# Optimization experiments

Measured on AMD Instinct MI355X. Metric: run time of the kernel, lower is better.

Reference implementation:

```python
import jax, jax.numpy as jnp
import numpy as np

B, N, H_DIM = 64, 128, 128
NODE_S, NODE_V = 64, 32            # irreps_node = 64x0e + 32x1o -> dim 160
OUT_S, OUT_V = 32, 16              # out irreps  = 32x0e + 16x1o -> dim 80
RBF, ZEMB, HID, LAT, EDIM, NE = 16, 32, 128, 256, 16, 512
EATT = 4096
CUTOFF = 5.0
MAXZ = 100
NODE_DIM = NODE_S + 3 * NODE_V
OUT_DIM = OUT_S + 3 * OUT_V
WN = NODE_S*OUT_S + NODE_V*OUT_S + NODE_S*OUT_V + NODE_V*OUT_V  # 4608 TP weights per edge
GATE_IN = H_DIM + H_DIM + RBF + 1

def _lin(k, fi, fo):
    return jax.random.normal(k, (fi, fo), jnp.float32) / np.sqrt(fi)

def setup_inputs() -> dict:
    ks = jax.random.split(jax.random.key(0), 24)
    flat = B * N
    att_dist = jax.random.uniform(ks[0], (EATT,), jnp.float32, 0.05, CUTOFF)
    dirs = jax.random.normal(ks[1], (EATT, 3), jnp.float32)
    dirs = dirs / jnp.linalg.norm(dirs, axis=-1, keepdims=True)
    return dict(
        h=jax.random.normal(ks[2], (B, N, H_DIM), jnp.float32),
        h_full=jax.random.normal(ks[3], (B, N, NODE_DIM), jnp.float32),
        z=jax.random.randint(ks[4], (B, N), 1, MAXZ + 1),
        mask=jnp.ones((B, N), bool),
        e_feat=jax.random.normal(ks[5], (NE, EDIM), jnp.float32),
        absorber_index=jax.random.randint(ks[6], (B,), 0, N),
        att_dst=jax.random.randint(ks[7], (EATT,), 0, flat),
        att_dist=att_dist,
        att_vec=dirs * att_dist[:, None],
        w_zemb=jax.random.normal(ks[8], (MAXZ + 1, ZEMB), jnp.float32),
        w1_rad=_lin(ks[9], ZEMB + 1 + RBF, HID), b1_rad=jnp.zeros(HID, jnp.float32),
        w2_rad=_lin(ks[10], HID, WN), b2_rad=jnp.zeros(WN, jnp.float32),
        wg1=_lin(ks[11], GATE_IN, HID), bg1=jnp.zeros(HID, jnp.float32),
        wg2=_lin(ks[12], HID, 1), bg2=jnp.zeros(1, jnp.float32),
        we1=_lin(ks[13], EDIM, HID), be1=jnp.zeros(HID, jnp.float32),
        we2=_lin(ks[14], HID, OUT_S + OUT_V), be2=jnp.ones(OUT_S + OUT_V, jnp.float32),
        wo1=_lin(ks[15], OUT_S + OUT_V, HID), bo1=jnp.zeros(HID, jnp.float32),
        wo2=_lin(ks[16], HID, HID), bo2=jnp.zeros(HID, jnp.float32),
        wo3=_lin(ks[17], HID, LAT), bo3=jnp.zeros(LAT, jnp.float32),
    )

def _core(h, h_full, z, e_feat, absorber_index, att_dst, att_dist, att_vec,
          w_zemb, w1_rad, b1_rad, w2_rad, b2_rad, wg1, bg1, wg2, bg2,
          we1, be1, we2, be2, wo1, bo1, wo2, bo2, wo3, bo3):
    B_, N_, H_ = h.shape
    flat = B_ * N_
    dt = h.dtype
    # scatter edge data into flat (B*N) buffers
    amask = jnp.zeros((flat,), bool).at[att_dst].set(True)
    dflat = jnp.zeros((flat,), dt).at[att_dst].set(att_dist.astype(dt))
    vflat = jnp.zeros((flat, 3), dt).at[att_dst].set(att_vec.astype(dt))
    eps = jnp.maximum(dflat, 1e-8)
    u = vflat / eps[:, None]
    # component-normalized real spherical harmonics, lmax=1: Y0 = 1, Y1 = sqrt(3)*u
    ys = jnp.ones((flat, 1), dt)
    yv = jnp.sqrt(jnp.asarray(3.0, dt)) * u
    # Gaussian RBF on distance
    centers = jnp.linspace(0.0, CUTOFF, RBF).astype(dt)
    width = CUTOFF / (RBF - 1)
    rbf = jnp.exp(-0.5 * ((dflat[:, None] - centers) / width) ** 2)
    zr = w_zemb[z].reshape(flat, ZEMB)
    is_abs = jax.nn.one_hot(absorber_index, N_, dtype=dt)  # (B,N)
    win = jnp.concatenate([zr, is_abs.reshape(flat, 1), rbf], -1)
    tpw = jax.nn.silu(win @ w1_rad + b1_rad) @ w2_rad + b2_rad  # (flat, WN)
    o = 0
    wA = tpw[:, o:o + NODE_S*OUT_S].reshape(flat, NODE_S, OUT_S); o += NODE_S*OUT_S
    wB = tpw[:, o:o + NODE_V*OUT_S].reshape(flat, NODE_V, OUT_S); o += NODE_V*OUT_S
    wC = tpw[:, o:o + NODE_S*OUT_V].reshape(flat, NODE_S, OUT_V); o += NODE_S*OUT_V
    wD = tpw[:, o:o + NODE_V*OUT_V].reshape(flat, NODE_V, OUT_V)
    hf = h_full.reshape(flat, NODE_DIM)
    s1 = hf[:, :NODE_S]
    v1 = hf[:, NODE_S:].reshape(flat, NODE_V, 3)
    norm = 1.0 / np.sqrt(NODE_S + NODE_V)   # TP path (fan-in) normalization
    inv_s3 = 1.0 / np.sqrt(3.0)             # CG(1,1->0) = delta/sqrt(3)
    out_s = (jnp.einsum('ei,eio->eo', s1 * ys, wA)
             + jnp.einsum('eic,ec,eio->eo', v1, yv, wB) * inv_s3) * norm
    out_v = (jnp.einsum('ei,eio->eo', s1, wC)[:, :, None] * yv[:, None, :]
             + jnp.einsum('eic,eio->eoc', v1, wD) * ys[:, :, None]) * norm
    ve = jnp.concatenate([out_s, out_v.reshape(flat, 3 * OUT_V)], -1)
    env = jnp.where(dflat < CUTOFF, 0.5 * (jnp.cos(np.pi * dflat / CUTOFF) + 1.0), 0.0)[:, None]
    ve = ve * env
    # PaiNN-style scalar edge gate
    h_abs = jnp.take_along_axis(h, absorber_index[:, None, None], axis=1)  # (B,1,H)
    gate_in = jnp.concatenate([jnp.broadcast_to(h_abs, (B_, N_, H_)), h,
                               rbf.reshape(B_, N_, RBF), is_abs[..., None]], -1)
    gate = jax.nn.sigmoid(jax.nn.silu(gate_in @ wg1 + bg1) @ wg2 + bg2).reshape(flat, 1)
    ve = ve * gate * amask[:, None].astype(dt)
    v_abs = ve.reshape(B_, N_, OUT_DIM).sum(1)  # (B, OUT_DIM)
    # energy irrep modulation: per-mul scalar from energy features
    scales = jax.nn.silu(e_feat @ we1 + be1) @ we2 + be2  # (nE, OUT_S+OUT_V)
    scale_full = jnp.concatenate([scales[:, :OUT_S], jnp.repeat(scales[:, OUT_S:], 3, axis=-1)], -1)
    v_mod = v_abs[:, None, :] * scale_full[None]  # (B, nE, OUT_DIM)
    vecs = v_mod[..., OUT_S:].reshape(B_, scales.shape[0], OUT_V, 3)
    inv = jnp.concatenate([v_mod[..., :OUT_S], jnp.sqrt(jnp.sum(vecs * vecs, -1) + 1e-12)], -1)
    x = jax.nn.silu(inv @ wo1 + bo1)
    x = jax.nn.silu(x @ wo2 + bo2)
    return x @ wo3 + bo3  # (B, nE, LAT)

def reference(h, h_full, z, mask, e_feat, absorber_index, att_dst, att_dist, att_vec,
              w_zemb, w1_rad, b1_rad, w2_rad, b2_rad, wg1, bg1, wg2, bg2,
              we1, be1, we2, be2, wo1, bo1, wo2, bo2, wo3, bo3):
    # mask is computed into att_mask in the original but never used downstream
    return _core(h, h_full, z, e_feat, absorber_index, att_dst, att_dist, att_vec,
                 w_zemb, w1_rad, b1_rad, w2_rad, b2_rad, wg1, bg1, wg2, bg2,
                 we1, be1, we2, be2, wo1, bo1, wo2, bo2, wo3, bo3)
```

## Files before the change

### kernel.cpp

```cpp
#include <hip/hip_runtime.h>
#include <math.h>

#define FLAT   8192
#define NB     64
#define OD_    80
#define NE_    512
#define EATT_  4096
#define MAXACT 4096
#define PARTW 1088

typedef __bf16 v8bf __attribute__((ext_vector_type(8)));
typedef float  v4f  __attribute__((ext_vector_type(4)));

__device__ __forceinline__ float silu_f(float x) { return x / (1.f + __expf(-x)); }
__device__ __forceinline__ float sigm_f(float x) { return 1.f / (1.f + __expf(-x)); }

__device__ __forceinline__ void transpose_split(const float* __restrict__ src, int ld,
                                                int nbase, __bf16* wh, __bf16* wl,
                                                float (*lds)[129]) {
  int t = threadIdx.x;
#pragma unroll
  for (int it = 0; it < 16; ++it) {
    int idx = it * 256 + t;
    int r = idx >> 5, c4 = idx & 31;
    float4 v = *(const float4*)(src + (size_t)r * ld + nbase + c4 * 4);
    lds[r][c4 * 4 + 0] = v.x;
    lds[r][c4 * 4 + 1] = v.y;
    lds[r][c4 * 4 + 2] = v.z;
    lds[r][c4 * 4 + 3] = v.w;
  }
  __syncthreads();
  int n = t >> 1, kh = (t & 1) * 64;
  union { __bf16 b[64]; uint4 u[8]; } H, L;
#pragma unroll
  for (int k = 0; k < 64; ++k) {
    float v = lds[kh + k][n];
    __bf16 hv = (__bf16)v;
    H.b[k] = hv;
    L.b[k] = (__bf16)(v - (float)hv);
  }
  uint4* ph = (uint4*)(wh + (size_t)(nbase + n) * 128 + kh);
  uint4* pl = (uint4*)(wl + (size_t)(nbase + n) * 128 + kh);
#pragma unroll
  for (int i = 0; i < 8; ++i) { ph[i] = H.u[i]; pl[i] = L.u[i]; }
}

__global__ __launch_bounds__(256) void k_prep(
    const float* __restrict__ w2_rad, const float* __restrict__ wo2,
    const float* __restrict__ wo3,
    const int* __restrict__ abs_idx, const float* __restrict__ h,
    const float* __restrict__ wg1,
    const float* __restrict__ e_feat,
    const float* __restrict__ we1, const float* __restrict__ be1,
    const float* __restrict__ we2, const float* __restrict__ be2,
    __bf16* w2rt_h, __bf16* w2rt_l, __bf16* w2t_h, __bf16* w2t_l,
    __bf16* w3t_h, __bf16* w3t_l,
    float* habs_g, float* vabs, int* widx, int* count, float* sfull) {
  __shared__ float lds[128][129];
  int bid = blockIdx.x;
  int t = threadIdx.x;
  if (bid < 36) {
    transpose_split(w2_rad, 4608, bid * 128, w2rt_h, w2rt_l, lds);
  } else if (bid < 37) {
    transpose_split(wo2, 128, 0, w2t_h, w2t_l, lds);
  } else if (bid < 39) {
    transpose_split(wo3, 256, (bid - 37) * 128, w3t_h, w3t_l, lds);
  } else if (bid < 71) {
    float* hs = &lds[0][0];
    int half = t >> 7, tt = t & 127;
    int b = (bid - 39) * 2 + half;
    int nabs = abs_idx[b];
    hs[half * 128 + tt] = h[(size_t)(b * 128 + nabs) * 128 + tt];
    __syncthreads();
    float g = 0.f;
    for (int c = 0; c < 128; ++c) g = fmaf(hs[half * 128 + c], wg1[c * 128 + tt], g);
    habs_g[b * 128 + tt] = g;
  } else if (bid < 103) {
    int g = (bid - 71) * 256 + t;
    if (g < FLAT) widx[g] = -1;
    if (g < NB * OD_) vabs[g] = 0.f;
    if (g == 0) *count = 0;
  } else {
    float* hid = &lds[0][0];
    int half = t >> 7, tt = t & 127;
    int row = (bid - 103) * 2 + half;
    const float* ef = e_feat + row * 16;
    float s = be1[tt];
    for (int k = 0; k < 16; ++k) s = fmaf(ef[k], we1[k * 128 + tt], s);
    hid[half * 128 + tt] = silu_f(s);
    __syncthreads();
    if (tt < 48) {
      float o = be2[tt];
      for (int k = 0; k < 128; ++k) o = fmaf(hid[half * 128 + k], we2[k * 48 + tt], o);
      if (tt < 32) sfull[row * 80 + tt] = o;
      else {
        int oo = tt - 32;
        sfull[row * 80 + 32 + oo * 3 + 0] = o;
        sfull[row * 80 + 32 + oo * 3 + 1] = o;
        sfull[row * 80 + 32 + oo * 3 + 2] = o;
      }
    }
  }
}

__global__ void k_scatter(const int* __restrict__ att_dst, int* widx) {
  int i = blockIdx.x * 256 + threadIdx.x;
  if (i < EATT_) atomicMax(&widx[att_dst[i]], i);
}

__global__ void k_build(const int* __restrict__ widx, int* active, int* count) {
  int j = blockIdx.x * 256 + threadIdx.x;
  if (j < FLAT && widx[j] >= 0) {
    int p = atomicAdd(count, 1);
    active[p] = j;
  }
}

__global__ __launch_bounds__(128) void k_node4(
    const int* __restrict__ count, const int* __restrict__ active,
    const int* __restrict__ widx,
    const float* __restrict__ att_dist, const float* __restrict__ att_vec,
    const int* __restrict__ z, const float* __restrict__ w_zemb,
    const int* __restrict__ abs_idx,
    const float* __restrict__ w1_rad, const float* __restrict__ b1_rad,
    const float* __restrict__ h, const float* __restrict__ habs_g,
    const float* __restrict__ wg1, const float* __restrict__ bg1,
    const float* __restrict__ wg2, const float* __restrict__ bg2,
    const float* __restrict__ h_full,
    __bf16* ah_glob, __bf16* al_glob,
    float* coef_glob, float* meta_f, int* meta_b) {
  int cnt = *count;
  int pbase = blockIdx.x * 4;
  if (pbase >= cnt) return;
  int t = threadIdx.x;

  __shared__ float win[4][49];
  __shared__ float yv_s[4][3];
  __shared__ float sh_d[4];
  __shared__ float red[4][128];
  __shared__ float hsh[4][128];

  bool ok[4];
  int jj[4], ee[4], bb[4];
  float isab[4];
#pragma unroll
  for (int q = 0; q < 4; ++q) {
    int pos = pbase + q;
    ok[q] = pos < cnt;
    jj[q] = ok[q] ? active[pos] : 0;
    ee[q] = ok[q] ? widx[jj[q]] : 0;
    if (ee[q] < 0) ee[q] = 0;
    bb[q] = jj[q] >> 7;
    isab[q] = ((jj[q] & 127) == abs_idx[bb[q]]) ? 1.f : 0.f;
  }

  if (t < 4) {
    int q = t;
    float d = att_dist[ee[q]];
    sh_d[q] = d;
    float eps = fmaxf(d, 1e-8f);
    const float s3 = 1.7320508075688772f;
    yv_s[q][0] = s3 * att_vec[ee[q] * 3 + 0] / eps;
    yv_s[q][1] = s3 * att_vec[ee[q] * 3 + 1] / eps;
    yv_s[q][2] = s3 * att_vec[ee[q] * 3 + 2] / eps;
  }
#pragma unroll
  for (int q = 0; q < 4; ++q) {
    if (t < 32) win[q][t] = w_zemb[z[jj[q]] * 32 + t];
    if (t == 32) win[q][32] = isab[q];
    if (t >= 33 && t < 49) {
      int k = t - 33;
      float d = att_dist[ee[q]];
      float x = (d - (float)k * (1.f / 3.f)) * 3.f;
      win[q][t] = __expf(-0.5f * x * x);
    }
    hsh[q][t] = h[(size_t)jj[q] * 128 + t];
  }
  __syncthreads();

  {
    float s[4];
    float bv = b1_rad[t];
#pragma unroll
    for (int q = 0; q < 4; ++q) s[q] = bv;
    for (int k = 0; k < 49; ++k) {
      float wv = w1_rad[k * 128 + t];
#pragma unroll
      for (int q = 0; q < 4; ++q) s[q] = fmaf(win[q][k], wv, s[q]);
    }
#pragma unroll
    for (int q = 0; q < 4; ++q) {
      if (ok[q]) {
        float av = silu_f(s[q]);
        __bf16 hv = (__bf16)av;
        ah_glob[(size_t)(pbase + q) * 128 + t] = hv;
        al_glob[(size_t)(pbase + q) * 128 + t] = (__bf16)(av - (float)hv);
      }
    }
  }

  {
    float g[4];
#pragma unroll
    for (int q = 0; q < 4; ++q) g[q] = bg1[t] + habs_g[bb[q] * 128 + t];
    for (int c = 0; c < 128; ++c) {
      float wv = wg1[(128 + c) * 128 + t];
#pragma unroll
      for (int q = 0; q < 4; ++q) g[q] = fmaf(hsh[q][c], wv, g[q]);
    }
    for (int k = 0; k < 16; ++k) {
      float wv = wg1[(256 + k) * 128 + t];
#pragma unroll
      for (int q = 0; q < 4; ++q) g[q] = fmaf(win[q][33 + k], wv, g[q]);
    }
    {
      float wv = wg1[272 * 128 + t];
#pragma unroll
      for (int q = 0; q < 4; ++q) g[q] = fmaf(isab[q], wv, g[q]);
    }
    float w2v = wg2[t];
#pragma unroll
    for (int q = 0; q < 4; ++q) red[q][t] = silu_f(g[q]) * w2v;
  }
  __syncthreads();

#pragma unroll
  for (int q = 0; q < 4; ++q) {
    if (!ok[q]) continue;
    int pos = pbase + q;
    const float* hf = h_full + (size_t)jj[q] * 160;
    if (t < 64) coef_glob[pos * 192 + t] = hf[t];
    if (t >= 64 && t < 96) {
      int i = t - 64;
      float pv = hf[64 + i * 3 + 0] * yv_s[q][0] + hf[64 + i * 3 + 1] * yv_s[q][1] +
                 hf[64 + i * 3 + 2] * yv_s[q][2];
      coef_glob[pos * 192 + t] = pv * 0.5773502691896258f;
    }
    if (t < 96) coef_glob[pos * 192 + 96 + t] = hf[64 + t];
  }

  if (t < 4) {
    int q = t;
    if (ok[q]) {
      int pos = pbase + q;
      float tot = 0.f;
      for (int k = 0; k < 128; ++k) tot += red[q][k];
      tot += bg2[0];
      float gate = sigm_f(tot);
      float d = sh_d[q];
      float env = (d < 5.f) ? 0.5f * (__cosf(3.14159265358979323846f * d * 0.2f) + 1.f) : 0.f;
      meta_f[pos * 4 + 0] = yv_s[q][0];
      meta_f[pos * 4 + 1] = yv_s[q][1];
      meta_f[pos * 4 + 2] = yv_s[q][2];
      meta_f[pos * 4 + 3] = gate * env;
      meta_b[pos] = bb[q];
    }
  }
}

__global__ __launch_bounds__(256) void k_mrgemm(
    const int* __restrict__ count,
    const __bf16* Ah, const __bf16* Al,
    const __bf16* __restrict__ Bh, const __bf16* __restrict__ Bl,
    const float* __restrict__ b2, const float* __restrict__ coef_glob,
    float* __restrict__ part) {
  int cc = blockIdx.x;
  int nbase = blockIdx.y * 128;
  int cnt = *count;
  if (nbase >= cnt) return;
  int t = threadIdx.x;
  int w = t >> 6, l = t & 63;
  int kg = l >> 4, ln = l & 15;
  int cbase = cc * 128;

  __shared__ v8bf Bs[2][2][8][64];

  size_t brow0 = (size_t)(cbase + w * 16 + ln) * 128 + kg * 8;
  size_t brow1 = (size_t)(cbase + (w + 4) * 16 + ln) * 128 + kg * 8;
  size_t arow0 = (size_t)(nbase + (2 * w) * 16 + ln) * 128 + kg * 8;
  size_t arow1 = (size_t)(nbase + (2 * w + 1) * 16 + ln) * 128 + kg * 8;

  v8bf rb0 = *(const v8bf*)(Bh + brow0);
  v8bf rb1 = *(const v8bf*)(Bh + brow1);
  v8bf rb2 = *(const v8bf*)(Bl + brow0);
  v8bf rb3 = *(const v8bf*)(Bl + brow1);
  v8bf ah0 = *(const v8bf*)(Ah + arow0);
  v8bf al0 = *(const v8bf*)(Al + arow0);
  v8bf ah1 = *(const v8bf*)(Ah + arow1);
  v8bf al1 = *(const v8bf*)(Al + arow1);
  Bs[0][0][w][l]     = rb0;
  Bs[0][0][w + 4][l] = rb1;
  Bs[0][1][w][l]     = rb2;
  Bs[0][1][w + 4][l] = rb3;
  __syncthreads();

  v4f acc[2][8];
  v4f z4 = {0.f, 0.f, 0.f, 0.f};
#pragma unroll
  for (int i = 0; i < 2; ++i)
#pragma unroll
    for (int j = 0; j < 8; ++j) acc[i][j] = z4;

  for (int kb = 0; kb < 4; ++kb) {
    int cur = kb & 1;
    v8bf nb0, nb1, nb2, nb3, nh0, nl0, nh1, nl1;
    if (kb < 3) {
      int off = (kb + 1) * 32;
      nb0 = *(const v8bf*)(Bh + brow0 + off);
      nb1 = *(const v8bf*)(Bh + brow1 + off);
      nb2 = *(const v8bf*)(Bl + brow0 + off);
      nb3 = *(const v8bf*)(Bl + brow1 + off);
      nh0 = *(const v8bf*)(Ah + arow0 + off);
      nl0 = *(const v8bf*)(Al + arow0 + off);
      nh1 = *(const v8bf*)(Ah + arow1 + off);
      nl1 = *(const v8bf*)(Al + arow1 + off);
    }
#pragma unroll
    for (int nt = 0; nt < 8; ++nt) {
      v8bf bh = Bs[cur][0][nt][l];
      v8bf bl = Bs[cur][1][nt][l];
      acc[0][nt] = __builtin_amdgcn_mfma_f32_16x16x32_bf16(ah0, bh, acc[0][nt], 0, 0, 0);
      acc[0][nt] = __builtin_amdgcn_mfma_f32_16x16x32_bf16(al0, bh, acc[0][nt], 0, 0, 0);
      acc[0][nt] = __builtin_amdgcn_mfma_f32_16x16x32_bf16(ah0, bl, acc[0][nt], 0, 0, 0);
      acc[1][nt] = __builtin_amdgcn_mfma_f32_16x16x32_bf16(ah1, bh, acc[1][nt], 0, 0, 0);
      acc[1][nt] = __builtin_amdgcn_mfma_f32_16x16x32_bf16(al1, bh, acc[1][nt], 0, 0, 0);
      acc[1][nt] = __builtin_amdgcn_mfma_f32_16x16x32_bf16(ah1, bl, acc[1][nt], 0, 0, 0);
    }
    if (kb < 3) {
      int nxt = cur ^ 1;
      Bs[nxt][0][w][l]     = nb0;
      Bs[nxt][0][w + 4][l] = nb1;
      Bs[nxt][1][w][l]     = nb2;
      Bs[nxt][1][w + 4][l] = nb3;
      ah0 = nh0; al0 = nl0; ah1 = nh1; al1 = nl1;
    }
    __syncthreads();
  }

  float b2v[8];
#pragma unroll
  for (int nt = 0; nt < 8; ++nt) b2v[nt] = b2[cbase + nt * 16 + ln];

#pragma unroll
  for (int mi = 0; mi < 2; ++mi) {
    int nodeb = nbase + (2 * w + mi) * 16 + kg * 4;
#pragma unroll
    for (int j = 0; j < 4; ++j) {
      int nd = nodeb + j;
      if (nd >= cnt) continue;
      const float* cf = coef_glob + (size_t)nd * 192;
      if (cc < 24) {
        float s0 = 0.f, s1 = 0.f;
#pragma unroll
        for (int m = 0; m < 4; ++m) {
          float c = cf[cc * 4 + m];
          s0 = fmaf(acc[mi][2 * m][j] + b2v[2 * m], c, s0);
          s1 = fmaf(acc[mi][2 * m + 1][j] + b2v[2 * m + 1], c, s1);
        }
        float* pp = part + (size_t)nd * PARTW + cc * 32 + ln;
        pp[0]  = s0;
        pp[16] = s1;
      } else if (cc < 32) {
        float s = 0.f;
#pragma unroll
        for (int nt = 0; nt < 8; ++nt)
          s = fmaf(acc[mi][nt][j] + b2v[nt], cf[(cc - 24) * 8 + nt], s);
        part[(size_t)nd * PARTW + 768 + (cc - 24) * 16 + ln] = s;
      } else {
        float s0 = 0.f, s1 = 0.f, s2 = 0.f;
#pragma unroll
        for (int nt = 0; nt < 8; ++nt) {
          float x = acc[mi][nt][j] + b2v[nt];
          const float* c3 = cf + 96 + ((cc - 32) * 8 + nt) * 3;
          s0 = fmaf(x, c3[0], s0);
          s1 = fmaf(x, c3[1], s1);
          s2 = fmaf(x, c3[2], s2);
        }
        float* pp = part + (size_t)nd * PARTW + 896 + (cc - 32) * 48 + ln;
        pp[0]  = s0;
        pp[16] = s1;
        pp[32] = s2;
      }
    }
  }
}

__global__ void k_combine(const int* __restrict__ count, const float* __restrict__ part,
                          const float* __restrict__ meta_f, const int* __restrict__ meta_b,
                          float* vabs) {
  int t = threadIdx.x;
  int pos = blockIdx.x * 2 + (t >> 7);
  int slot = t & 127;
  if (pos >= *count || slot >= 96) return;
  const float* pp = part + (size_t)pos * PARTW;
  float s = 0.f;
  if (slot < 32) {
#pragma unroll
    for (int c = 0; c < 24; ++c) s += pp[c * 32 + slot];
  } else if (slot < 48) {
#pragma unroll
    for (int c = 0; c < 8; ++c) s += pp[768 + c * 16 + (slot - 32)];
  } else {
#pragma unroll
    for (int c = 0; c < 4; ++c) s += pp[896 + c * 48 + (slot - 48)];
  }
  float sc = meta_f[pos * 4 + 3] * 0.10206207261596577f;
  float* vb = vabs + meta_b[pos] * 80;
  if (slot < 32) {
    unsafeAtomicAdd(&vb[slot], s * sc);
  } else if (slot < 48) {
    int o = slot - 32;
    float q = s * sc;
    unsafeAtomicAdd(&vb[32 + o * 3 + 0], q * meta_f[pos * 4 + 0]);
    unsafeAtomicAdd(&vb[32 + o * 3 + 1], q * meta_f[pos * 4 + 1]);
    unsafeAtomicAdd(&vb[32 + o * 3 + 2], q * meta_f[pos * 4 + 2]);
  } else {
    int s2 = slot - 48;
    int comp = s2 >> 4, o = s2 & 15;
    unsafeAtomicAdd(&vb[32 + o * 3 + comp], s * sc);
  }
}

__global__ __launch_bounds__(256) void k_head(
    const float* __restrict__ vabs, const float* __restrict__ sfull,
    const float* __restrict__ wo1, const float* __restrict__ bo1,
    const __bf16* __restrict__ W2h, const __bf16* __restrict__ W2l,
    const float* __restrict__ bo2,
    const __bf16* __restrict__ W3h, const __bf16* __restrict__ W3l,
    const float* __restrict__ bo3,
    float* __restrict__ out) {
  __shared__ __align__(16) char arena[69632];
  float* w_s = (float*)arena;
  float (*invt)[64] = (float(*)[64])(arena + 24576);
  float* va = (float*)(arena + 36864);
  char* xsh = arena;
  char* xsl = arena + 16384;
  v8bf (*BsB)[2][8][64] = (v8bf(*)[2][8][64])(arena + 36864);
  char* ysh = arena + 36864;
  char* ysl = arena + 53248;
  v8bf (*BsC)[2][8][64] = (v8bf(*)[2][8][64])arena;

  int rbase = blockIdx.x * 64;
  int b = rbase >> 9;
  int e0 = rbase & 511;
  int t = threadIdx.x;

  {
    int tx = t & 15, ty = t >> 4;
    int n0 = ty * 4;
    if (t < 80) va[t] = vabs[b * 80 + t];
    {
      const float4* wg = (const float4*)wo1;
      float4* ws4 = (float4*)w_s;
#pragma unroll
      for (int it = 0; it < 6; ++it) ws4[t + it * 256] = wg[t + it * 256];
    }
    __syncthreads();

    for (int idx = t; idx < 48 * 64; idx += 256) {
      int cd = idx >> 6, r = idx & 63;
      const float* sf = sfull + (size_t)(e0 + r) * 80;
      float v;
      if (cd < 32) v = va[cd] * sf[cd];
      else {
        int base = 32 + (cd - 32) * 3;
        float m0 = va[base + 0] * sf[base + 0];
        float m1 = va[base + 1] * sf[base + 1];
        float m2 = va[base + 2] * sf[base + 2];
        v = sqrtf(m0 * m0 + m1 * m1 + m2 * m2 + 1e-12f);
      }
      invt[cd][r] = v;
    }
    __syncthreads();

    float acc[4][8];
#pragma unroll
    for (int i = 0; i < 4; ++i)
#pragma unroll
      for (int j = 0; j < 8; ++j) acc[i][j] = 0.f;

    for (int k = 0; k < 48; ++k) {
      float4 av  = *(const float4*)&invt[k][n0];
      float4 w0  = *(const float4*)&w_s[k * 128 + tx * 4];
      float4 w1v = *(const float4*)&w_s[k * 128 + 64 + tx * 4];
#pragma unroll
      for (int i = 0; i < 4; ++i) {
        float a = (i == 0) ? av.x : (i == 1) ? av.y : (i == 2) ? av.z : av.w;
        acc[i][0] = fmaf(a, w0.x,  acc[i][0]);
        acc[i][1] = fmaf(a, w0.y,  acc[i][1]);
        acc[i][2] = fmaf(a, w0.z,  acc[i][2]);
        acc[i][3] = fmaf(a, w0.w,  acc[i][3]);
        acc[i][4] = fmaf(a, w1v.x, acc[i][4]);
        acc[i][5] = fmaf(a, w1v.y, acc[i][5]);
        acc[i][6] = fmaf(a, w1v.z, acc[i][6]);
        acc[i][7] = fmaf(a, w1v.w, acc[i][7]);
      }
    }
    __syncthreads();

    float4 bq0 = *(const float4*)(bo1 + tx * 4);
    float4 bq1 = *(const float4*)(bo1 + 64 + tx * 4);
#pragma unroll
    for (int i = 0; i < 4; ++i) {
      int row = n0 + i;
      int sw = (row & 7) << 4;
      float q0[4] = {silu_f(acc[i][0] + bq0.x), silu_f(acc[i][1] + bq0.y),
                     silu_f(acc[i][2] + bq0.z), silu_f(acc[i][3] + bq0.w)};
      float q1[4] = {silu_f(acc[i][4] + bq1.x), silu_f(acc[i][5] + bq1.y),
                     silu_f(acc[i][6] + bq1.z), silu_f(acc[i][7] + bq1.w)};
      union { __bf16 bb[4]; uint2 u; } H, L;
#pragma unroll
      for (int e = 0; e < 4; ++e) {
        __bf16 hv = (__bf16)q0[e];
        H.bb[e] = hv;
        L.bb[e] = (__bf16)(q0[e] - (float)hv);
      }
      *(uint2*)(xsh + ((row * 256 + tx * 8) ^ sw)) = H.u;
      *(uint2*)(xsl + ((row * 256 + tx * 8) ^ sw)) = L.u;
#pragma unroll
      for (int e = 0; e < 4; ++e) {
        __bf16 hv = (__bf16)q1[e];
        H.bb[e] = hv;
        L.bb[e] = (__bf16)(q1[e] - (float)hv);
      }
      *(uint2*)(xsh + ((row * 256 + 128 + tx * 8) ^ sw)) = H.u;
      *(uint2*)(xsl + ((row * 256 + 128 + tx * 8) ^ sw)) = L.u;
    }
  }
  __syncthreads();

  int w = t >> 6, l = t & 63;
  int kg = l >> 4, ln = l & 15;
  {
    int arw = w * 16 + ln;
    int sw = (arw & 7) << 4;
    v8bf axh[4], axl[4];
#pragma unroll
    for (int kb = 0; kb < 4; ++kb) {
      int byt = arw * 256 + kb * 64 + kg * 16;
      axh[kb] = *(v8bf*)(xsh + (byt ^ sw));
      axl[kb] = *(v8bf*)(xsl + (byt ^ sw));
    }
    {
      size_t p0 = (size_t)(w * 16 + ln) * 128 + kg * 8;
      size_t p1 = (size_t)((w + 4) * 16 + ln) * 128 + kg * 8;
      BsB[0][0][w][l]     = *(const v8bf*)(W2h + p0);
      BsB[0][0][w + 4][l] = *(const v8bf*)(W2h + p1);
      BsB[0][1][w][l]     = *(const v8bf*)(W2l + p0);
      BsB[0][1][w + 4][l] = *(const v8bf*)(W2l + p1);
    }
    __syncthreads();

    v4f acc[8];
    v4f z4 = {0.f, 0.f, 0.f, 0.f};
#pragma unroll
    for (int i = 0; i < 8; ++i) acc[i] = z4;

#pragma unroll
    for (int kb = 0; kb < 4; ++kb) {
      int cur = kb & 1;
      v8bf r0, r1, r2, r3;
      if (kb < 3) {
        size_t p0 = (size_t)(w * 16 + ln) * 128 + (kb + 1) * 32 + kg * 8;
        size_t p1 = (size_t)((w + 4) * 16 + ln) * 128 + (kb + 1) * 32 + kg * 8;
        r0 = *(const v8bf*)(W2h + p0);
        r1 = *(const v8bf*)(W2h + p1);
        r2 = *(const v8bf*)(W2l + p0);
        r3 = *(const v8bf*)(W2l + p1);
      }
#pragma unroll
      for (int nt = 0; nt < 8; ++nt) {
        v8bf bh = BsB[cur][0][nt][l];
        v8bf bl = BsB[cur][1][nt][l];
        acc[nt] = __builtin_amdgcn_mfma_f32_16x16x32_bf16(axh[kb], bh, acc[nt], 0, 0, 0);
        acc[nt] = __builtin_amdgcn_mfma_f32_16x16x32_bf16(axl[kb], bh, acc[nt], 0, 0, 0);
        acc[nt] = __builtin_amdgcn_mfma_f32_16x16x32_bf16(axh[kb], bl, acc[nt], 0, 0, 0);
      }
      if (kb < 3) {
        int nxt = cur ^ 1;
        BsB[nxt][0][w][l]     = r0;
        BsB[nxt][0][w + 4][l] = r1;
        BsB[nxt][1][w][l]     = r2;
        BsB[nxt][1][w + 4][l] = r3;
      }
      __syncthreads();
    }

    int r0l = w * 16 + kg * 4;
#pragma unroll
    for (int nt = 0; nt < 8; ++nt) {
      float bv = bo2[nt * 16 + ln];
#pragma unroll
      for (int j = 0; j < 4; ++j) {
        float x = silu_f(acc[nt][j] + bv);
        int row = r0l + j;
        int byt = (row * 256 + (nt * 16 + ln) * 2) ^ ((row & 7) << 4);
        __bf16 hv = (__bf16)x;
        *(__bf16*)(ysh + byt) = hv;
        *(__bf16*)(ysl + byt) = (__bf16)(x - (float)hv);
      }
    }
  }
  __syncthreads();

  {
    int arw = w * 16 + ln;
    int sw = (arw & 7) << 4;
    v8bf ayh[4], ayl[4];
#pragma unroll
    for (int kb = 0; kb < 4; ++kb) {
      int byt = arw * 256 + kb * 64 + kg * 16;
      ayh[kb] = *(v8bf*)(ysh + (byt ^ sw));
      ayl[kb] = *(v8bf*)(ysl + (byt ^ sw));
    }
    __syncthreads();

    for (int ch = 0; ch < 2; ++ch) {
      int cbase = ch * 128;
      {
        size_t p0 = (size_t)(cbase + w * 16 + ln) * 128 + kg * 8;
        size_t p1 = (size_t)(cbase + (w + 4) * 16 + ln) * 128 + kg * 8;
        BsC[0][0][w][l]     = *(const v8bf*)(W3h + p0);
        BsC[0][0][w + 4][l] = *(const v8bf*)(W3h + p1);
        BsC[0][1][w][l]     = *(const v8bf*)(W3l + p0);
        BsC[0][1][w + 4][l] = *(const v8bf*)(W3l + p1);
      }
      __syncthreads();

      v4f acc[8];
      v4f z4 = {0.f, 0.f, 0.f, 0.f};
#pragma unroll
      for (int i = 0; i < 8; ++i) acc[i] = z4;

#pragma unroll
      for (int kb = 0; kb < 4; ++kb) {
        int cur = kb & 1;
        v8bf r0, r1, r2, r3;
        if (kb < 3) {
          size_t p0 = (size_t)(cbase + w * 16 + ln) * 128 + (kb + 1) * 32 + kg * 8;
          size_t p1 = (size_t)(cbase + (w + 4) * 16 + ln) * 128 + (kb + 1) * 32 + kg * 8;
          r0 = *(const v8bf*)(W3h + p0);
          r1 = *(const v8bf*)(W3h + p1);
          r2 = *(const v8bf*)(W3l + p0);
          r3 = *(const v8bf*)(W3l + p1);
        }
#pragma unroll
        for (int nt = 0; nt < 8; ++nt) {
          v8bf bh = BsC[cur][0][nt][l];
          v8bf bl = BsC[cur][1][nt][l];
          acc[nt] = __builtin_amdgcn_mfma_f32_16x16x32_bf16(ayh[kb], bh, acc[nt], 0, 0, 0);
          acc[nt] = __builtin_amdgcn_mfma_f32_16x16x32_bf16(ayl[kb], bh, acc[nt], 0, 0, 0);
          acc[nt] = __builtin_amdgcn_mfma_f32_16x16x32_bf16(ayh[kb], bl, acc[nt], 0, 0, 0);
        }
        if (kb < 3) {
          int nxt = cur ^ 1;
          BsC[nxt][0][w][l]     = r0;
          BsC[nxt][0][w + 4][l] = r1;
          BsC[nxt][1][w][l]     = r2;
          BsC[nxt][1][w + 4][l] = r3;
        }
        __syncthreads();
      }

      int r0g = rbase + w * 16 + kg * 4;
#pragma unroll
      for (int nt = 0; nt < 8; ++nt) {
        float bv = bo3[cbase + nt * 16 + ln];
#pragma unroll
        for (int j = 0; j < 4; ++j) {
          out[(size_t)(r0g + j) * 256 + cbase + nt * 16 + ln] = acc[nt][j] + bv;
        }
      }
    }
  }
}

extern "C" void kernel_launch(void* const* d_in, const int* in_sizes, int n_in,
                              void* d_out, int out_size, void* d_ws, size_t ws_size,
                              hipStream_t stream) {
  const float* h        = (const float*)d_in[0];
  const float* h_full   = (const float*)d_in[1];
  const int*   z        = (const int*)d_in[2];
  const float* e_feat   = (const float*)d_in[4];
  const int*   abs_idx  = (const int*)d_in[5];
  const int*   att_dst  = (const int*)d_in[6];
  const float* att_dist = (const float*)d_in[7];
  const float* att_vec  = (const float*)d_in[8];
  const float* w_zemb   = (const float*)d_in[9];
  const float* w1_rad   = (const float*)d_in[10];
  const float* b1_rad   = (const float*)d_in[11];
  const float* w2_rad   = (const float*)d_in[12];
  const float* b2_rad   = (const float*)d_in[13];
  const float* wg1      = (const float*)d_in[14];
  const float* bg1      = (const float*)d_in[15];
  const float* wg2      = (const float*)d_in[16];
  const float* bg2      = (const float*)d_in[17];
  const float* we1      = (const float*)d_in[18];
  const float* be1      = (const float*)d_in[19];
  const float* we2      = (const float*)d_in[20];
  const float* be2      = (const float*)d_in[21];
  const float* wo1      = (const float*)d_in[22];
  const float* bo1      = (const float*)d_in[23];
  const float* wo2      = (const float*)d_in[24];
  const float* bo2      = (const float*)d_in[25];
  const float* wo3      = (const float*)d_in[26];
  const float* bo3      = (const float*)d_in[27];
  float* out = (float*)d_out;

  float* meta_f  = (float*)d_ws;
  float* vabs    = meta_f + MAXACT * 4;
  float* sfull   = vabs + NB * OD_;
  float* habs_g  = sfull + NE_ * OD_;
  __bf16* w2t_h  = (__bf16*)(habs_g + NB * 128);
  __bf16* w2t_l  = w2t_h + 128 * 128;
  __bf16* w3t_h  = w2t_l + 128 * 128;
  __bf16* w3t_l  = w3t_h + 256 * 128;
  int* widx   = (int*)(w3t_l + 256 * 128);
  int* active = widx + FLAT;
  int* meta_b = active + MAXACT;
  int* count  = meta_b + MAXACT;
  float* big  = (float*)(count + 15);
  __bf16* ah_glob  = (__bf16*)big;
  __bf16* al_glob  = ah_glob + MAXACT * 128;
  float* coef_glob = (float*)(al_glob + MAXACT * 128);
  __bf16* w2rt_h   = (__bf16*)(coef_glob + MAXACT * 192);
  __bf16* w2rt_l   = w2rt_h + 4608 * 128;
  float* part      = (float*)(w2rt_l + 4608 * 128);

  k_prep<<<359, 256, 0, stream>>>(w2_rad, wo2, wo3, abs_idx, h, wg1,
                                  e_feat, we1, be1, we2, be2,
                                  w2rt_h, w2rt_l, w2t_h, w2t_l, w3t_h, w3t_l,
                                  habs_g, vabs, widx, count, sfull);
  k_scatter<<<16, 256, 0, stream>>>(att_dst, widx);
  k_build<<<32, 256, 0, stream>>>(widx, active, count);
  k_node4<<<1024, 128, 0, stream>>>(count, active, widx, att_dist, att_vec, z, w_zemb,
                                    abs_idx, w1_rad, b1_rad, h, habs_g, wg1, bg1, wg2, bg2,
                                    h_full, ah_glob, al_glob, coef_glob, meta_f, meta_b);
  k_mrgemm<<<dim3(36, 32), 256, 0, stream>>>(count, ah_glob, al_glob, w2rt_h, w2rt_l,
                                             b2_rad, coef_glob, part);
  k_combine<<<2048, 256, 0, stream>>>(count, part, meta_f, meta_b, vabs);
  k_head<<<512, 256, 0, stream>>>(vabs, sfull, wo1, bo1, w2t_h, w2t_l, bo2,
                                  w3t_h, w3t_l, bo3, out);
}
```

Measured before the change: 216.0 us.

## Remove combine kernel by atomically accumulating GEMM partials and reducing in head

The GEMM epilogue now atomically adds its per-column-chunk partial sums into a compact 96-wide per-node accumulator instead of writing a 1088-wide partial buffer. The separate combine kernel is removed. Each head block instead gathers its batch's active nodes through a new inverse index and applies the gate scale and direction to build v_abs in shared memory. This saves one launch and the large partial-buffer round trip. In exchange it adds atomic contention in the GEMM and redundant per-batch reduction work in each of the 8 head blocks that share a batch.

```diff
diff --git a/kernel.cpp b/kernel.cpp
--- a/kernel.cpp
+++ b/kernel.cpp
@@ -7,7 +7,7 @@
 #define NE_    512
 #define EATT_  4096
 #define MAXACT 4096
-#define PARTW 1088
+#define ACCW 96
 
 typedef __bf16 v8bf __attribute__((ext_vector_type(8)));
 typedef float  v4f  __attribute__((ext_vector_type(4)));
@@ -55,7 +55,7 @@
     const float* __restrict__ we2, const float* __restrict__ be2,
     __bf16* w2rt_h, __bf16* w2rt_l, __bf16* w2t_h, __bf16* w2t_l,
     __bf16* w3t_h, __bf16* w3t_l,
-    float* habs_g, float* vabs, int* widx, int* count, float* sfull) {
+    float* habs_g, float* acc_glob, int* widx, int* count, float* sfull) {
   __shared__ float lds[128][129];
   int bid = blockIdx.x;
   int t = threadIdx.x;
@@ -77,9 +77,12 @@
     habs_g[b * 128 + tt] = g;
   } else if (bid < 103) {
     int g = (bid - 71) * 256 + t;
-    if (g < FLAT) widx[g] = -1;
-    if (g < NB * OD_) vabs[g] = 0.f;
+    widx[g] = -1;
     if (g == 0) *count = 0;
+    float4* ap = (float4*)(acc_glob + (size_t)g * 48);
+    float4 z = make_float4(0.f, 0.f, 0.f, 0.f);
+#pragma unroll
+    for (int i = 0; i < 12; ++i) ap[i] = z;
   } else {
     float* hid = &lds[0][0];
     int half = t >> 7, tt = t & 127;
@@ -108,11 +111,12 @@
   if (i < EATT_) atomicMax(&widx[att_dst[i]], i);
 }
 
-__global__ void k_build(const int* __restrict__ widx, int* active, int* count) {
+__global__ void k_build(const int* __restrict__ widx, int* active, int* inv, int* count) {
   int j = blockIdx.x * 256 + threadIdx.x;
   if (j < FLAT && widx[j] >= 0) {
     int p = atomicAdd(count, 1);
     active[p] = j;
+    inv[j] = p;
   }
 }
 
@@ -128,7 +132,7 @@
     const float* __restrict__ wg2, const float* __restrict__ bg2,
     const float* __restrict__ h_full,
     __bf16* ah_glob, __bf16* al_glob,
-    float* coef_glob, float* meta_f, int* meta_b) {
+    float* coef_glob, float* meta_f) {
   int cnt = *count;
   int pbase = blockIdx.x * 4;
   if (pbase >= cnt) return;
@@ -253,7 +257,6 @@
       meta_f[pos * 4 + 1] = yv_s[q][1];
       meta_f[pos * 4 + 2] = yv_s[q][2];
       meta_f[pos * 4 + 3] = gate * env;
-      meta_b[pos] = bb[q];
     }
   }
 }
@@ -263,7 +266,7 @@
     const __bf16* Ah, const __bf16* Al,
     const __bf16* __restrict__ Bh, const __bf16* __restrict__ Bl,
     const float* __restrict__ b2, const float* __restrict__ coef_glob,
-    float* __restrict__ part) {
+    float* __restrict__ acc_glob) {
   int cc = blockIdx.x;
   int nbase = blockIdx.y * 128;
   int cnt = *count;
@@ -349,6 +352,7 @@
       int nd = nodeb + j;
       if (nd >= cnt) continue;
       const float* cf = coef_glob + (size_t)nd * 192;
+      float* dst = acc_glob + (size_t)nd * ACCW;
       if (cc < 24) {
         float s0 = 0.f, s1 = 0.f;
 #pragma unroll
@@ -357,15 +361,14 @@
           s0 = fmaf(acc[mi][2 * m][j] + b2v[2 * m], c, s0);
           s1 = fmaf(acc[mi][2 * m + 1][j] + b2v[2 * m + 1], c, s1);
         }
-        float* pp = part + (size_t)nd * PARTW + cc * 32 + ln;
-        pp[0]  = s0;
-        pp[16] = s1;
+        unsafeAtomicAdd(&dst[ln], s0);
+        unsafeAtomicAdd(&dst[16 + ln], s1);
       } else if (cc < 32) {
         float s = 0.f;
 #pragma unroll
         for (int nt = 0; nt < 8; ++nt)
           s = fmaf(acc[mi][nt][j] + b2v[nt], cf[(cc - 24) * 8 + nt], s);
-        part[(size_t)nd * PARTW + 768 + (cc - 24) * 16 + ln] = s;
+        unsafeAtomicAdd(&dst[32 + ln], s);
       } else {
         float s0 = 0.f, s1 = 0.f, s2 = 0.f;
 #pragma unroll
@@ -376,53 +379,18 @@
           s1 = fmaf(x, c3[1], s1);
           s2 = fmaf(x, c3[2], s2);
         }
-        float* pp = part + (size_t)nd * PARTW + 896 + (cc - 32) * 48 + ln;
-        pp[0]  = s0;
-        pp[16] = s1;
-        pp[32] = s2;
+        unsafeAtomicAdd(&dst[48 + ln], s0);
+        unsafeAtomicAdd(&dst[48 + 16 + ln], s1);
+        unsafeAtomicAdd(&dst[48 + 32 + ln], s2);
       }
     }
   }
 }
 
-__global__ void k_combine(const int* __restrict__ count, const float* __restrict__ part,
-                          const float* __restrict__ meta_f, const int* __restrict__ meta_b,
-                          float* vabs) {
-  int t = threadIdx.x;
-  int pos = blockIdx.x * 2 + (t >> 7);
-  int slot = t & 127;
-  if (pos >= *count || slot >= 96) return;
-  const float* pp = part + (size_t)pos * PARTW;
-  float s = 0.f;
-  if (slot < 32) {
-#pragma unroll
-    for (int c = 0; c < 24; ++c) s += pp[c * 32 + slot];
-  } else if (slot < 48) {
-#pragma unroll
-    for (int c = 0; c < 8; ++c) s += pp[768 + c * 16 + (slot - 32)];
-  } else {
-#pragma unroll
-    for (int c = 0; c < 4; ++c) s += pp[896 + c * 48 + (slot - 48)];
-  }
-  float sc = meta_f[pos * 4 + 3] * 0.10206207261596577f;
-  float* vb = vabs + meta_b[pos] * 80;
-  if (slot < 32) {
-    unsafeAtomicAdd(&vb[slot], s * sc);
-  } else if (slot < 48) {
-    int o = slot - 32;
-    float q = s * sc;
-    unsafeAtomicAdd(&vb[32 + o * 3 + 0], q * meta_f[pos * 4 + 0]);
-    unsafeAtomicAdd(&vb[32 + o * 3 + 1], q * meta_f[pos * 4 + 1]);
-    unsafeAtomicAdd(&vb[32 + o * 3 + 2], q * meta_f[pos * 4 + 2]);
-  } else {
-    int s2 = slot - 48;
-    int comp = s2 >> 4, o = s2 & 15;
-    unsafeAtomicAdd(&vb[32 + o * 3 + comp], s * sc);
-  }
-}
-
 __global__ __launch_bounds__(256) void k_head(
-    const float* __restrict__ vabs, const float* __restrict__ sfull,
+    const int* __restrict__ widx, const int* __restrict__ inv,
+    const float* __restrict__ meta_f, const float* __restrict__ acc_glob,
+    const float* __restrict__ sfull,
     const float* __restrict__ wo1, const float* __restrict__ bo1,
     const __bf16* __restrict__ W2h, const __bf16* __restrict__ W2l,
     const float* __restrict__ bo2,
@@ -433,6 +401,7 @@
   float* w_s = (float*)arena;
   float (*invt)[64] = (float(*)[64])(arena + 24576);
   float* va = (float*)(arena + 36864);
+  float (*pgrp)[80] = (float(*)[80])(arena + 36864 + 320);
   char* xsh = arena;
   char* xsl = arena + 16384;
   v8bf (*BsB)[2][8][64] = (v8bf(*)[2][8][64])(arena + 36864);
@@ -446,16 +415,38 @@
   int t = threadIdx.x;
 
   {
+    const float4* wg = (const float4*)wo1;
+    float4* ws4 = (float4*)w_s;
+#pragma unroll
+    for (int it = 0; it < 6; ++it) ws4[t + it * 256] = wg[t + it * 256];
+
+    if (t < 240) {
+      int slot = t % 80, grp = t / 80;
+      float s = 0.f;
+      for (int idx = grp; idx < 128; idx += 3) {
+        int j = (b << 7) + idx;
+        if (widx[j] < 0) continue;
+        int pos = inv[j];
+        float sc = meta_f[pos * 4 + 3] * 0.10206207261596577f;
+        const float* ac = acc_glob + (size_t)pos * ACCW;
+        if (slot < 32) {
+          s = fmaf(ac[slot], sc, s);
+        } else {
+          int o = (slot - 32) / 3, comp = (slot - 32) % 3;
+          s = fmaf(ac[32 + o], sc * meta_f[pos * 4 + comp], s);
+          s = fmaf(ac[48 + comp * 16 + o], sc, s);
+        }
+      }
+      pgrp[grp][slot] = s;
+    }
+  }
+  __syncthreads();
+  if (t < 80) va[t] = pgrp[0][t] + pgrp[1][t] + pgrp[2][t];
+  __syncthreads();
+
+  {
     int tx = t & 15, ty = t >> 4;
     int n0 = ty * 4;
-    if (t < 80) va[t] = vabs[b * 80 + t];
-    {
-      const float4* wg = (const float4*)wo1;
-      float4* ws4 = (float4*)w_s;
-#pragma unroll
-      for (int it = 0; it < 6; ++it) ws4[t + it * 256] = wg[t + it * 256];
-    }
-    __syncthreads();
 
     for (int idx = t; idx < 48 * 64; idx += 256) {
       int cd = idx >> 6, r = idx & 63;
@@ -708,8 +699,7 @@
   float* out = (float*)d_out;
 
   float* meta_f  = (float*)d_ws;
-  float* vabs    = meta_f + MAXACT * 4;
-  float* sfull   = vabs + NB * OD_;
+  float* sfull   = meta_f + MAXACT * 4;
   float* habs_g  = sfull + NE_ * OD_;
   __bf16* w2t_h  = (__bf16*)(habs_g + NB * 128);
   __bf16* w2t_l  = w2t_h + 128 * 128;
@@ -717,28 +707,27 @@
   __bf16* w3t_l  = w3t_h + 256 * 128;
   int* widx   = (int*)(w3t_l + 256 * 128);
   int* active = widx + FLAT;
-  int* meta_b = active + MAXACT;
-  int* count  = meta_b + MAXACT;
-  float* big  = (float*)(count + 15);
+  int* inv    = active + MAXACT;
+  int* count  = inv + FLAT;
+  float* big  = (float*)(((size_t)(count + 1) + 255) & ~(size_t)255);
   __bf16* ah_glob  = (__bf16*)big;
   __bf16* al_glob  = ah_glob + MAXACT * 128;
   float* coef_glob = (float*)(al_glob + MAXACT * 128);
   __bf16* w2rt_h   = (__bf16*)(coef_glob + MAXACT * 192);
   __bf16* w2rt_l   = w2rt_h + 4608 * 128;
-  float* part      = (float*)(w2rt_l + 4608 * 128);
+  float* acc_glob  = (float*)(w2rt_l + 4608 * 128);
 
   k_prep<<<359, 256, 0, stream>>>(w2_rad, wo2, wo3, abs_idx, h, wg1,
                                   e_feat, we1, be1, we2, be2,
                                   w2rt_h, w2rt_l, w2t_h, w2t_l, w3t_h, w3t_l,
-                                  habs_g, vabs, widx, count, sfull);
+                                  habs_g, acc_glob, widx, count, sfull);
   k_scatter<<<16, 256, 0, stream>>>(att_dst, widx);
-  k_build<<<32, 256, 0, stream>>>(widx, active, count);
+  k_build<<<32, 256, 0, stream>>>(widx, active, inv, count);
   k_node4<<<1024, 128, 0, stream>>>(count, active, widx, att_dist, att_vec, z, w_zemb,
                                     abs_idx, w1_rad, b1_rad, h, habs_g, wg1, bg1, wg2, bg2,
-                                    h_full, ah_glob, al_glob, coef_glob, meta_f, meta_b);
+                                    h_full, ah_glob, al_glob, coef_glob, meta_f);
   k_mrgemm<<<dim3(36, 32), 256, 0, stream>>>(count, ah_glob, al_glob, w2rt_h, w2rt_l,
-                                             b2_rad, coef_glob, part);
-  k_combine<<<2048, 256, 0, stream>>>(count, part, meta_f, meta_b, vabs);
-  k_head<<<512, 256, 0, stream>>>(vabs, sfull, wo1, bo1, w2t_h, w2t_l, bo2,
-                                  w3t_h, w3t_l, bo3, out);
+                                             b2_rad, coef_glob, acc_glob);
+  k_head<<<512, 256, 0, stream>>>(widx, inv, meta_f, acc_glob, sfull, wo1, bo1,
+                                  w2t_h, w2t_l, bo2, w3t_h, w3t_l, bo3, out);
 }
```

New measurement: 242.9 us. 12.5% more time.
